# Kernel optimization log

Measured on AMD Instinct MI355X. Metric: run time of the kernel, lower is better.

## Reference

```python
import jax, jax.numpy as jnp
import numpy as np

B, T, D, O = 8, 128, 512, 512


def setup_inputs() -> dict:
    key = jax.random.key(0)
    ks = jax.random.split(key, 10)
    w = 0.02  # small init scale, mimics GlorotNormal magnitude
    return {
        "inputs": jax.random.normal(ks[0], (B, T, D), dtype=jnp.float32),
        "Wa": jax.random.normal(ks[1], (O, O), dtype=jnp.float32) * w,
        "Ua": jax.random.normal(ks[2], (D, O), dtype=jnp.float32) * w,
        "Va": jax.random.normal(ks[3], (O, 1), dtype=jnp.float32) * w,
        "Ba": jax.random.normal(ks[4], (1, O), dtype=jnp.float32) * w,
        "Wo": jax.random.normal(ks[5], (O, 1), dtype=jnp.float32) * w,
        "Uo": jax.random.normal(ks[6], (D, O), dtype=jnp.float32) * w,
        "Co": jax.random.normal(ks[7], (D, O), dtype=jnp.float32) * w,
        "Bo": jax.random.normal(ks[8], (1, O), dtype=jnp.float32) * w,
        "emb": jax.random.normal(ks[9], (O, O), dtype=jnp.float32) * w,
    }


def reference(inputs, Wa, Ua, Va, Ba, Wo, Uo, Co, Bo, emb):
    # inputs: [B,T,D]. Precompute loop-invariant attention keys (incl. Ba).
    UaH = jnp.einsum('btd,do->bto', inputs, Ua) + Ba  # [B,T,O]
    # GRU 'prev_state' arg at step t is inputs[:, t-1, :] (t=0 -> last step).
    prev_h = jnp.roll(inputs, 1, axis=1)              # [B,T,D]
    xs = jnp.swapaxes(prev_h, 0, 1)                   # [T,B,D]
    b, o = inputs.shape[0], Wa.shape[0]

    def step(prev_pred, h_prev):
        # --- attention cell (query = sigmoid(prev_pred)) ---
        s = jax.nn.sigmoid(prev_pred)                  # [B,O]
        WaS = s @ Wa                                   # [B,O]
        e = jnp.tanh(UaH + WaS[:, None, :])            # [B,T,O]
        scores = jnp.squeeze(e @ Va, -1)               # [B,T]
        sm = jax.nn.softmax(scores, axis=1)            # softmax over timesteps
        ctx = jnp.einsum('bt,btd->bd', sm, inputs)     # [B,D]
        # --- cascaded GRU cell ---
        emb_out = jax.nn.softmax(prev_pred, axis=-1) @ emb  # [B,O]
        WoY = emb_out @ Wo                             # [B,1] (broadcasts over O)
        pred = WoY + h_prev @ Uo + ctx @ Co + Bo       # [B,O]
        return pred, pred

    init = jnp.zeros((b, o), dtype=inputs.dtype)
    _, out = jax.lax.scan(step, init, xs)              # [T,B,O]
    return jnp.swapaxes(out, 0, 1)                     # [B,T,O]
```

## Files before the change

kernel.cpp:

```cpp
#include <hip/hip_runtime.h>

#define L2E 1.44269504088896340736f


__device__ __forceinline__ float ld_agent(float* p) {
  return __hip_atomic_load(p, __ATOMIC_RELAXED, __HIP_MEMORY_SCOPE_AGENT);
}
__device__ __forceinline__ void st_agent(float* p, float v) {
  __hip_atomic_store(p, v, __ATOMIC_RELAXED, __HIP_MEMORY_SCOPE_AGENT);
}

__device__ __forceinline__ void group_barrier(int* cnt, int target) {
  __syncthreads();
  if (threadIdx.x == 0) {
    __hip_atomic_fetch_add(cnt, 1, __ATOMIC_RELEASE, __HIP_MEMORY_SCOPE_AGENT);
    while (__hip_atomic_load(cnt, __ATOMIC_ACQUIRE, __HIP_MEMORY_SCOPE_AGENT) < target) { }
  }
  __syncthreads();
}

__global__ __launch_bounds__(256) void gemm_pre(
    const float* __restrict__ A, const float* __restrict__ Ua,
    const float* __restrict__ Uo, const float* __restrict__ Co,
    float* __restrict__ XW)
{
  __shared__ float sA[64][33];
  __shared__ float sB[32][68];
  const int r0 = blockIdx.x * 64;
  const int c0 = blockIdx.y * 64;
  const float* Wm; int cc0;
  if (c0 < 512)       { Wm = Ua; cc0 = c0; }
  else if (c0 < 1024) { Wm = Uo; cc0 = c0 - 512; }
  else                { Wm = Co; cc0 = c0 - 1024; }
  const int tid = threadIdx.x;
  const int ty4 = (tid >> 4) * 4;
  const int tx4 = (tid & 15) * 4;
  float acc[4][4] = {};
  for (int k0 = 0; k0 < 512; k0 += 32) {
    for (int t4 = tid; t4 < 512; t4 += 256) {
      int row = t4 >> 3, kq = (t4 & 7) << 2;
      float4 v = *reinterpret_cast<const float4*>(&A[(size_t)(r0 + row) * 512 + k0 + kq]);
      sA[row][kq] = v.x; sA[row][kq + 1] = v.y; sA[row][kq + 2] = v.z; sA[row][kq + 3] = v.w;
    }
    for (int t4 = tid; t4 < 512; t4 += 256) {
      int kk = t4 >> 4, cq = (t4 & 15) << 2;
      float4 v = *reinterpret_cast<const float4*>(&Wm[(size_t)(k0 + kk) * 512 + cc0 + cq]);
      sB[kk][cq] = v.x; sB[kk][cq + 1] = v.y; sB[kk][cq + 2] = v.z; sB[kk][cq + 3] = v.w;
    }
    __syncthreads();
    #pragma unroll 8
    for (int kk = 0; kk < 32; ++kk) {
      float a0 = sA[ty4 + 0][kk], a1 = sA[ty4 + 1][kk];
      float a2 = sA[ty4 + 2][kk], a3 = sA[ty4 + 3][kk];
      float4 bv = *reinterpret_cast<const float4*>(&sB[kk][tx4]);
      acc[0][0] += a0 * bv.x; acc[0][1] += a0 * bv.y; acc[0][2] += a0 * bv.z; acc[0][3] += a0 * bv.w;
      acc[1][0] += a1 * bv.x; acc[1][1] += a1 * bv.y; acc[1][2] += a1 * bv.z; acc[1][3] += a1 * bv.w;
      acc[2][0] += a2 * bv.x; acc[2][1] += a2 * bv.y; acc[2][2] += a2 * bv.z; acc[2][3] += a2 * bv.w;
      acc[3][0] += a3 * bv.x; acc[3][1] += a3 * bv.y; acc[3][2] += a3 * bv.z; acc[3][3] += a3 * bv.w;
    }
    __syncthreads();
  }
  for (int i = 0; i < 4; ++i) {
    float4 v = make_float4(acc[i][0], acc[i][1], acc[i][2], acc[i][3]);
    *reinterpret_cast<float4*>(&XW[(size_t)(r0 + ty4 + i) * 1536 + c0 + tx4]) = v;
  }
}

__global__ __launch_bounds__(512) void embwo_kernel(
    const float* __restrict__ emb, const float* __restrict__ Wo,
    float* __restrict__ gEmbWo)
{
  const int lane = threadIdx.x & 63;
  const int wv = threadIdx.x >> 6;
  const int kbase = blockIdx.x * 64 + wv * 8;
  for (int i = 0; i < 8; ++i) {
    const int k = kbase + i;
    float acc = 0.f;
    #pragma unroll
    for (int c = 0; c < 8; ++c) {
      int o = lane + 64 * c;
      acc += emb[(size_t)k * 512 + o] * Wo[o];
    }
    #pragma unroll
    for (int d = 1; d < 64; d <<= 1) acc += __shfl_xor(acc, d);
    if (lane == 0) gEmbWo[k] = acc;
  }
}

__global__ __launch_bounds__(512) void coop_scan(
    const float* __restrict__ Wa, const float* __restrict__ Va,
    const float* __restrict__ Ba, const float* __restrict__ Bo,
    const float* __restrict__ gXW, const float* __restrict__ gEmbWo,
    float* gPred, float* gSP, int* cnt, float* __restrict__ out)
{
  extern __shared__ float smem[];
  float* sWa     = smem;
  float* sUaH    = smem + 16384;
  float* sICo    = smem + 20480;
  float* sP1     = smem + 24576;
  float* sS      = smem + 28672;
  float* sEmbWo  = smem + 29184;
  float* sRed    = smem + 29696;
  float* sScores = smem + 30208;
  float* sSm     = smem + 30336;
  float* sVa     = smem + 30464;
  float* sWaS    = smem + 30496;

  const int tid = threadIdx.x;
  const int lane = tid & 63;
  const int wv = tid >> 6;
  const int b = blockIdx.x & 7;
  const int j = blockIdx.x >> 3;
  const int obase = j * 32;
  int* bcnt = cnt + b;

  for (int idx = tid; idx < 512 * 32; idx += 512) {
    int k = idx >> 5, oo = idx & 31;
    sWa[idx] = Wa[(size_t)k * 512 + obase + oo];
  }
  for (int idx = tid; idx < 128 * 32; idx += 512) {
    int tt = idx >> 5, oo = idx & 31;
    int col = obase + oo;
    const float* rowp = gXW + (size_t)(b * 128 + tt) * 1536;
    sUaH[idx] = rowp[col] + Ba[col];
    sICo[idx] = rowp[1024 + col];
    int tprev = (tt + 127) & 127;
    sP1[idx] = gXW[(size_t)(b * 128 + tprev) * 1536 + 512 + col] + Bo[col];
  }
  if (tid < 32) sVa[tid] = Va[obase + tid];
  sEmbWo[tid] = gEmbWo[tid];
  __syncthreads();

  float p = 0.f;
  int bseq = 0;

  for (int t = 0; t < 128; ++t) {
    sS[tid] = 1.f / (1.f + exp2f(-p * L2E));
    float m = p;
    #pragma unroll
    for (int d = 1; d < 64; d <<= 1) m = fmaxf(m, __shfl_xor(m, d));
    if (lane == 0) sRed[wv] = m;
    __syncthreads();
    float mm = sRed[0];
    #pragma unroll
    for (int i = 1; i < 8; ++i) mm = fmaxf(mm, sRed[i]);
    float ee = exp2f((p - mm) * L2E);
    float dd = ee * sEmbWo[tid];
    #pragma unroll
    for (int d = 1; d < 64; d <<= 1) { ee += __shfl_xor(ee, d); dd += __shfl_xor(dd, d); }
    if (lane == 0) { sRed[8 + wv] = ee; sRed[16 + wv] = dd; }
    __syncthreads();
    float den = 0.f, num = 0.f;
    #pragma unroll
    for (int i = 0; i < 8; ++i) { den += sRed[8 + i]; num += sRed[16 + i]; }
    const float WoY = num / den;
    __syncthreads();

    {
      const int kg = tid >> 5, oo = tid & 31;
      const int kb = kg * 32;
      float acc = 0.f;
      #pragma unroll 8
      for (int i = 0; i < 32; ++i) acc += sS[kb + i] * sWa[(size_t)(kb + i) * 32 + oo];
      sRed[tid] = acc;
    }
    __syncthreads();
    if (tid < 32) {
      float w = 0.f;
      #pragma unroll
      for (int g = 0; g < 16; ++g) w += sRed[g * 32 + tid];
      sWaS[tid] = w;
    }
    __syncthreads();

    {
      const int tp = tid >> 2, q = tid & 3;
      const float4* ua4 = reinterpret_cast<const float4*>(sUaH + tp * 32 + q * 8);
      float4 u0 = ua4[0], u1 = ua4[1];
      float uu[8] = {u0.x, u0.y, u0.z, u0.w, u1.x, u1.y, u1.z, u1.w};
      float acc = 0.f;
      #pragma unroll
      for (int i = 0; i < 8; ++i) {
        const int o = q * 8 + i;
        float u = uu[i] + sWaS[o];
        float ex = exp2f(u * (2.f * L2E));
        float th = 1.f - 2.f / (1.f + ex);
        acc += th * sVa[o];
      }
      acc += __shfl_xor(acc, 1);
      acc += __shfl_xor(acc, 2);
      if (q == 0) st_agent(gSP + (size_t)(b * 16 + j) * 128 + tp, acc);
    }
    ++bseq; group_barrier(bcnt, 16 * bseq);

    if (tid < 128) {
      float sc = 0.f;
      #pragma unroll
      for (int i = 0; i < 16; ++i) sc += ld_agent(gSP + (size_t)(b * 16 + i) * 128 + tid);
      sScores[tid] = sc;
    }
    __syncthreads();
    float v = (tid < 128) ? sScores[tid] : -1e30f;
    float mt = v;
    #pragma unroll
    for (int d = 1; d < 64; d <<= 1) mt = fmaxf(mt, __shfl_xor(mt, d));
    if (lane == 0) sRed[wv] = mt;
    __syncthreads();
    float mm2 = fmaxf(sRed[0], sRed[1]);
    float ev = (tid < 128) ? exp2f((v - mm2) * L2E) : 0.f;
    float sv = ev;
    #pragma unroll
    for (int d = 1; d < 64; d <<= 1) sv += __shfl_xor(sv, d);
    if (lane == 0) sRed[8 + wv] = sv;
    __syncthreads();
    float dsum = sRed[8] + sRed[9];
    if (tid < 128) sSm[tid] = ev / dsum;
    __syncthreads();

    {
      const int tg = tid >> 5, oo = tid & 31;
      const int tb = tg * 8;
      float acc = 0.f;
      #pragma unroll
      for (int i = 0; i < 8; ++i) acc += sSm[tb + i] * sICo[(size_t)(tb + i) * 32 + oo];
      sRed[tid] = acc;
    }
    __syncthreads();
    if (tid < 32) {
      float c = 0.f;
      #pragma unroll
      for (int g = 0; g < 16; ++g) c += sRed[g * 32 + tid];
      float pr = WoY + sP1[t * 32 + tid] + c;
      out[(size_t)(b * 128 + t) * 512 + obase + tid] = pr;
      st_agent(gPred + b * 512 + obase + tid, pr);
    }
    ++bseq; group_barrier(bcnt, 16 * bseq);
    p = ld_agent(gPred + b * 512 + tid);
  }
}

extern "C" void kernel_launch(void* const* d_in, const int* in_sizes, int n_in,
                              void* d_out, int out_size, void* d_ws, size_t ws_size,
                              hipStream_t stream)
{
  const float* inputs = (const float*)d_in[0];
  const float* Wa  = (const float*)d_in[1];
  const float* Ua  = (const float*)d_in[2];
  const float* Va  = (const float*)d_in[3];
  const float* Ba  = (const float*)d_in[4];
  const float* Wo  = (const float*)d_in[5];
  const float* Uo  = (const float*)d_in[6];
  const float* Co  = (const float*)d_in[7];
  const float* Bo  = (const float*)d_in[8];
  const float* emb = (const float*)d_in[9];
  float* out = (float*)d_out;

  char* ws = (char*)d_ws;
  int*   cnt    = (int*)(ws + 0);
  float* gPred  = (float*)(ws + 256);
  float* gSP    = (float*)(ws + 16896);
  float* gEmbWo = (float*)(ws + 82432);
  float* gXW    = (float*)(ws + 131072);

  hipMemsetAsync(d_ws, 0, 16640, stream);

  dim3 gg(16, 24);
  gemm_pre<<<gg, 256, 0, stream>>>(inputs, Ua, Uo, Co, gXW);
  embwo_kernel<<<8, 512, 0, stream>>>(emb, Wo, gEmbWo);

  const int smem_bytes = 30528 * 4;
  hipFuncSetAttribute((const void*)coop_scan,
                      hipFuncAttributeMaxDynamicSharedMemorySize, smem_bytes);
  coop_scan<<<128, 512, smem_bytes, stream>>>(Wa, Va, Ba, Bo, gXW, gEmbWo,
                                              gPred, gSP, cnt, out);
}
```

Measured before the change: 1.365 ms.

## Halve scan block size, double-buffer exchange slots, drop max-subtraction in softmaxes

The persistent recurrent scan kernel now runs 256 threads per block instead of 512. It uses separate cache-line-padded counters for the score and prediction barriers, and parity double-buffered exchange slots. Both softmaxes skip the max reduction, which removes several block-wide syncs per step, and the attention keys are transposed in shared memory to avoid bank conflicts. Fewer threads mean more serial work per thread, and softmax without max subtraction is only safe because pred and score magnitudes stay small.

```diff
diff --git a/kernel.cpp b/kernel.cpp
--- a/kernel.cpp
+++ b/kernel.cpp
@@ -3,20 +3,11 @@
 #define L2E 1.44269504088896340736f
 
 
-__device__ __forceinline__ float ld_agent(float* p) {
+__device__ __forceinline__ float ld_agent(const float* p) {
   return __hip_atomic_load(p, __ATOMIC_RELAXED, __HIP_MEMORY_SCOPE_AGENT);
 }
 __device__ __forceinline__ void st_agent(float* p, float v) {
   __hip_atomic_store(p, v, __ATOMIC_RELAXED, __HIP_MEMORY_SCOPE_AGENT);
-}
-
-__device__ __forceinline__ void group_barrier(int* cnt, int target) {
-  __syncthreads();
-  if (threadIdx.x == 0) {
-    __hip_atomic_fetch_add(cnt, 1, __ATOMIC_RELEASE, __HIP_MEMORY_SCOPE_AGENT);
-    while (__hip_atomic_load(cnt, __ATOMIC_ACQUIRE, __HIP_MEMORY_SCOPE_AGENT) < target) { }
-  }
-  __syncthreads();
 }
 
 __global__ __launch_bounds__(256) void gemm_pre(
@@ -87,24 +78,25 @@
   }
 }
 
-__global__ __launch_bounds__(512) void coop_scan(
+__global__ __launch_bounds__(256) void coop_scan(
     const float* __restrict__ Wa, const float* __restrict__ Va,
     const float* __restrict__ Ba, const float* __restrict__ Bo,
     const float* __restrict__ gXW, const float* __restrict__ gEmbWo,
-    float* gPred, float* gSP, int* cnt, float* __restrict__ out)
+    float* slotP, float* slotS, int* cntS, int* cntP, float* __restrict__ out)
 {
   extern __shared__ float smem[];
-  float* sWa     = smem;
-  float* sUaH    = smem + 16384;
-  float* sICo    = smem + 20480;
-  float* sP1     = smem + 24576;
-  float* sS      = smem + 28672;
-  float* sEmbWo  = smem + 29184;
-  float* sRed    = smem + 29696;
-  float* sScores = smem + 30208;
-  float* sSm     = smem + 30336;
-  float* sVa     = smem + 30464;
-  float* sWaS    = smem + 30496;
+  float* sWa   = smem;
+  float* sUaHT = smem + 16384;
+  float* sICo  = smem + 20512;
+  float* sP1   = smem + 24608;
+  float* sPred = smem + 28704;
+  float* sS    = smem + 29216;
+  float* sEmb  = smem + 29728;
+  float* sVa   = smem + 30240;
+  float* sWaS  = smem + 30272;
+  float* sSm   = smem + 30304;
+  float* sRedB = smem + 30432;
+  float* sRed  = smem + 30688;
 
   const int tid = threadIdx.x;
   const int lane = tid & 63;
@@ -112,130 +104,120 @@
   const int b = blockIdx.x & 7;
   const int j = blockIdx.x >> 3;
   const int obase = j * 32;
-  int* bcnt = cnt + b;
-
-  for (int idx = tid; idx < 512 * 32; idx += 512) {
+  int* mycntS = cntS + b * 64;
+  int* mycntP = cntP + b * 64;
+
+  for (int idx = tid; idx < 512 * 32; idx += 256) {
     int k = idx >> 5, oo = idx & 31;
     sWa[idx] = Wa[(size_t)k * 512 + obase + oo];
   }
-  for (int idx = tid; idx < 128 * 32; idx += 512) {
+  for (int idx = tid; idx < 128 * 32; idx += 256) {
     int tt = idx >> 5, oo = idx & 31;
     int col = obase + oo;
     const float* rowp = gXW + (size_t)(b * 128 + tt) * 1536;
-    sUaH[idx] = rowp[col] + Ba[col];
-    sICo[idx] = rowp[1024 + col];
+    sUaHT[oo * 129 + tt] = rowp[col] + Ba[col];
+    sICo[tt * 32 + oo] = rowp[1024 + col];
     int tprev = (tt + 127) & 127;
-    sP1[idx] = gXW[(size_t)(b * 128 + tprev) * 1536 + 512 + col] + Bo[col];
+    sP1[tt * 32 + oo] = gXW[(size_t)(b * 128 + tprev) * 1536 + 512 + col] + Bo[col];
   }
   if (tid < 32) sVa[tid] = Va[obase + tid];
-  sEmbWo[tid] = gEmbWo[tid];
-  __syncthreads();
-
-  float p = 0.f;
-  int bseq = 0;
+  sEmb[tid] = gEmbWo[tid]; sEmb[tid + 256] = gEmbWo[tid + 256];
+  sPred[tid] = 0.f; sPred[tid + 256] = 0.f;
 
   for (int t = 0; t < 128; ++t) {
-    sS[tid] = 1.f / (1.f + exp2f(-p * L2E));
-    float m = p;
+    __syncthreads();
+
+    float p1 = sPred[tid], p2 = sPred[tid + 256];
+    sS[tid]       = 1.f / (1.f + exp2f(-p1 * L2E));
+    sS[tid + 256] = 1.f / (1.f + exp2f(-p2 * L2E));
+    float e1 = exp2f(p1 * L2E), e2 = exp2f(p2 * L2E);
+    float Ep = e1 + e2;
+    float Dp = e1 * sEmb[tid] + e2 * sEmb[tid + 256];
     #pragma unroll
-    for (int d = 1; d < 64; d <<= 1) m = fmaxf(m, __shfl_xor(m, d));
-    if (lane == 0) sRed[wv] = m;
-    __syncthreads();
-    float mm = sRed[0];
-    #pragma unroll
-    for (int i = 1; i < 8; ++i) mm = fmaxf(mm, sRed[i]);
-    float ee = exp2f((p - mm) * L2E);
-    float dd = ee * sEmbWo[tid];
-    #pragma unroll
-    for (int d = 1; d < 64; d <<= 1) { ee += __shfl_xor(ee, d); dd += __shfl_xor(dd, d); }
-    if (lane == 0) { sRed[8 + wv] = ee; sRed[16 + wv] = dd; }
-    __syncthreads();
-    float den = 0.f, num = 0.f;
-    #pragma unroll
-    for (int i = 0; i < 8; ++i) { den += sRed[8 + i]; num += sRed[16 + i]; }
-    const float WoY = num / den;
-    __syncthreads();
+    for (int d = 1; d < 64; d <<= 1) { Ep += __shfl_xor(Ep, d); Dp += __shfl_xor(Dp, d); }
+    if (lane == 0) { sRed[wv] = Ep; sRed[4 + wv] = Dp; }
+    __syncthreads();
+    const float WoY = (sRed[4] + sRed[5] + sRed[6] + sRed[7])
+                    / (sRed[0] + sRed[1] + sRed[2] + sRed[3]);
 
     {
-      const int kg = tid >> 5, oo = tid & 31;
-      const int kb = kg * 32;
+      const int o = tid & 31, kg = tid >> 5, kb = kg * 64;
       float acc = 0.f;
-      #pragma unroll 8
-      for (int i = 0; i < 32; ++i) acc += sS[kb + i] * sWa[(size_t)(kb + i) * 32 + oo];
-      sRed[tid] = acc;
+      #pragma unroll 16
+      for (int i = 0; i < 64; ++i) acc += sS[kb + i] * sWa[(kb + i) * 32 + o];
+      sRedB[kg * 32 + o] = acc;
     }
     __syncthreads();
     if (tid < 32) {
       float w = 0.f;
       #pragma unroll
-      for (int g = 0; g < 16; ++g) w += sRed[g * 32 + tid];
+      for (int g = 0; g < 8; ++g) w += sRedB[g * 32 + tid];
       sWaS[tid] = w;
     }
     __syncthreads();
 
     {
-      const int tp = tid >> 2, q = tid & 3;
-      const float4* ua4 = reinterpret_cast<const float4*>(sUaH + tp * 32 + q * 8);
-      float4 u0 = ua4[0], u1 = ua4[1];
-      float uu[8] = {u0.x, u0.y, u0.z, u0.w, u1.x, u1.y, u1.z, u1.w};
+      const int h = tid & 1, tp = tid >> 1;
       float acc = 0.f;
       #pragma unroll
-      for (int i = 0; i < 8; ++i) {
-        const int o = q * 8 + i;
-        float u = uu[i] + sWaS[o];
+      for (int i = 0; i < 16; ++i) {
+        const int oo = h * 16 + i;
+        float u = sUaHT[oo * 129 + tp] + sWaS[oo];
         float ex = exp2f(u * (2.f * L2E));
-        float th = 1.f - 2.f / (1.f + ex);
-        acc += th * sVa[o];
+        acc += (1.f - 2.f / (1.f + ex)) * sVa[oo];
       }
       acc += __shfl_xor(acc, 1);
-      acc += __shfl_xor(acc, 2);
-      if (q == 0) st_agent(gSP + (size_t)(b * 16 + j) * 128 + tp, acc);
-    }
-    ++bseq; group_barrier(bcnt, 16 * bseq);
+      if (h == 0) st_agent(slotS + (((t & 1) * 8 + b) * 16 + j) * 128 + tp, acc);
+    }
+    __syncthreads();
+    if (tid == 0) {
+      __hip_atomic_fetch_add(mycntS, 1, __ATOMIC_RELEASE, __HIP_MEMORY_SCOPE_AGENT);
+      const int tgt = 16 * (t + 1);
+      while (__hip_atomic_load(mycntS, __ATOMIC_ACQUIRE, __HIP_MEMORY_SCOPE_AGENT) < tgt) { }
+    }
+    __syncthreads();
 
     if (tid < 128) {
+      const float* basep = slotS + ((t & 1) * 8 + b) * 2048 + tid;
       float sc = 0.f;
       #pragma unroll
-      for (int i = 0; i < 16; ++i) sc += ld_agent(gSP + (size_t)(b * 16 + i) * 128 + tid);
-      sScores[tid] = sc;
-    }
-    __syncthreads();
-    float v = (tid < 128) ? sScores[tid] : -1e30f;
-    float mt = v;
-    #pragma unroll
-    for (int d = 1; d < 64; d <<= 1) mt = fmaxf(mt, __shfl_xor(mt, d));
-    if (lane == 0) sRed[wv] = mt;
-    __syncthreads();
-    float mm2 = fmaxf(sRed[0], sRed[1]);
-    float ev = (tid < 128) ? exp2f((v - mm2) * L2E) : 0.f;
-    float sv = ev;
-    #pragma unroll
-    for (int d = 1; d < 64; d <<= 1) sv += __shfl_xor(sv, d);
-    if (lane == 0) sRed[8 + wv] = sv;
-    __syncthreads();
-    float dsum = sRed[8] + sRed[9];
-    if (tid < 128) sSm[tid] = ev / dsum;
-    __syncthreads();
+      for (int jj = 0; jj < 16; ++jj) sc += ld_agent(basep + jj * 128);
+      float ev = exp2f(sc * L2E);
+      sSm[tid] = ev;
+      float sv = ev;
+      #pragma unroll
+      for (int d = 1; d < 64; d <<= 1) sv += __shfl_xor(sv, d);
+      if (lane == 0) sRed[8 + wv] = sv;
+    }
+    __syncthreads();
+    const float rden = 1.f / (sRed[8] + sRed[9]);
 
     {
-      const int tg = tid >> 5, oo = tid & 31;
-      const int tb = tg * 8;
+      const int o = tid & 31, g = tid >> 5, tb = g * 16;
       float acc = 0.f;
       #pragma unroll
-      for (int i = 0; i < 8; ++i) acc += sSm[tb + i] * sICo[(size_t)(tb + i) * 32 + oo];
-      sRed[tid] = acc;
+      for (int i = 0; i < 16; ++i) acc += sSm[tb + i] * sICo[(tb + i) * 32 + o];
+      sRedB[g * 32 + o] = acc;
     }
     __syncthreads();
     if (tid < 32) {
       float c = 0.f;
       #pragma unroll
-      for (int g = 0; g < 16; ++g) c += sRed[g * 32 + tid];
-      float pr = WoY + sP1[t * 32 + tid] + c;
+      for (int g2 = 0; g2 < 8; ++g2) c += sRedB[g2 * 32 + tid];
+      float pr = WoY + sP1[t * 32 + tid] + c * rden;
       out[(size_t)(b * 128 + t) * 512 + obase + tid] = pr;
-      st_agent(gPred + b * 512 + obase + tid, pr);
-    }
-    ++bseq; group_barrier(bcnt, 16 * bseq);
-    p = ld_agent(gPred + b * 512 + tid);
+      st_agent(slotP + ((t & 1) * 8 + b) * 512 + obase + tid, pr);
+    }
+    __syncthreads();
+    if (tid == 0) {
+      __hip_atomic_fetch_add(mycntP, 1, __ATOMIC_RELEASE, __HIP_MEMORY_SCOPE_AGENT);
+      const int tgt = 16 * (t + 1);
+      while (__hip_atomic_load(mycntP, __ATOMIC_ACQUIRE, __HIP_MEMORY_SCOPE_AGENT) < tgt) { }
+    }
+    __syncthreads();
+    const float* pp = slotP + ((t & 1) * 8 + b) * 512;
+    sPred[tid] = ld_agent(pp + tid);
+    sPred[tid + 256] = ld_agent(pp + tid + 256);
   }
 }
 
@@ -256,21 +238,22 @@
   float* out = (float*)d_out;
 
   char* ws = (char*)d_ws;
-  int*   cnt    = (int*)(ws + 0);
-  float* gPred  = (float*)(ws + 256);
-  float* gSP    = (float*)(ws + 16896);
-  float* gEmbWo = (float*)(ws + 82432);
+  int*   cntS   = (int*)(ws + 0);
+  int*   cntP   = (int*)(ws + 2048);
+  float* slotP  = (float*)(ws + 8192);
+  float* slotS  = (float*)(ws + 40960);
+  float* gEmbWo = (float*)(ws + 106496);
   float* gXW    = (float*)(ws + 131072);
 
-  hipMemsetAsync(d_ws, 0, 16640, stream);
+  hipMemsetAsync(d_ws, 0, 4096, stream);
 
   dim3 gg(16, 24);
   gemm_pre<<<gg, 256, 0, stream>>>(inputs, Ua, Uo, Co, gXW);
   embwo_kernel<<<8, 512, 0, stream>>>(emb, Wo, gEmbWo);
 
-  const int smem_bytes = 30528 * 4;
+  const int smem_bytes = 30704 * 4;
   hipFuncSetAttribute((const void*)coop_scan,
                       hipFuncAttributeMaxDynamicSharedMemorySize, smem_bytes);
-  coop_scan<<<128, 512, smem_bytes, stream>>>(Wa, Va, Ba, Bo, gXW, gEmbWo,
-                                              gPred, gSP, cnt, out);
-}
+  coop_scan<<<128, 256, smem_bytes, stream>>>(Wa, Va, Ba, Bo, gXW, gEmbWo,
+                                              slotP, slotS, cntS, cntP, out);
+}
```

Result: faster. 1.334 ms (-2.3%).
